# Kernel optimization log

Measured on AMD Instinct MI355X. Metric: run time of the kernel, lower is better.

## Reference

```python
import jax, jax.numpy as jnp
import numpy as np

H, W = 512, 512
N = H * W
NCLS = 4
D_BI, D_SP = 5, 2
THETA_ALPHA, THETA_BETA, THETA_GAMMA = 80.0, 0.0625, 3.0
BI_COMPAT, SP_COMPAT, COMPATIBILITY = 10.0, 3.0, -1.0
NUM_ITER = 10


def _build_lattice(feats):
    """Permutohedral lattice precompute (numpy, integer index construction).
    feats: [N, d]. Returns os [N,d+1] int32 (1-based), ws [N,d+1] float32,
    bn [d+1, M, 2] int32 (0 = missing neighbor), M."""
    feats = np.asarray(feats, np.float64)
    n, d = feats.shape
    inv_std = np.sqrt(2.0 / 3.0) * (d + 1)
    scale = inv_std / np.sqrt((np.arange(d) + 1.0) * (np.arange(d) + 2.0))
    cf = feats * scale
    # embedding matrix E: elevated = cf @ E.T lies on the hyperplane sum=0
    E = np.zeros((d + 1, d))
    E[0, :] = 1.0
    for j in range(1, d + 1):
        E[j, j:] = 1.0
        E[j, j - 1] = -j
    elevated = cf @ E.T  # [n, d+1]
    greedy = (np.rint(elevated / (d + 1)) * (d + 1)).astype(np.int64)
    diff = elevated - greedy
    idx = np.arange(d + 1)
    upper = idx[None, :] > idx[:, None]
    lower = idx[None, :] < idx[:, None]
    di = diff[:, :, None]
    dj = diff[:, None, :]
    rank = (((dj > di) & upper) | ((dj >= di) & lower)).sum(-1)
    rank = rank + greedy.sum(1, keepdims=True) // (d + 1)
    low = rank < 0
    rank = rank + np.where(low, d + 1, 0)
    greedy = greedy + np.where(low, d + 1, 0)
    high = rank > d
    rank = rank - np.where(high, d + 1, 0)
    greedy = greedy - np.where(high, d + 1, 0)
    # barycentric weights
    bary = np.zeros((n, d + 2))
    v = (elevated - greedy) / (d + 1)
    rows = np.repeat(np.arange(n), d + 1)
    np.add.at(bary, (rows, (d - rank).ravel()), v.ravel())
    np.add.at(bary, (rows, (d + 1 - rank).ravel()), -v.ravel())
    bary[:, 0] += 1.0 + bary[:, d + 1]
    ws = bary[:, : d + 1].astype(np.float32)
    # simplex vertex keys (first d coords; last is implied by zero-sum)
    keys = np.empty((n, d + 1, d), np.int64)
    for r in range(d + 1):
        keys[:, r, :] = (greedy + r - (d + 1) * (rank > d - r))[:, :d]
    flat = keys.reshape(-1, d)
    lo = flat.min(0) - (d + 1)
    hi = flat.max(0) + (d + 1)
    strides = np.cumprod(np.concatenate([[1], (hi - lo + 1)[:-1]]))
    coords = (flat - lo) @ strides
    uniq, first, inv = np.unique(coords, return_index=True, return_inverse=True)
    M = int(len(uniq))
    os_ = (inv.reshape(n, d + 1) + 1).astype(np.int32)
    ukeys = flat[first]
    bn = np.zeros((d + 1, M, 2), np.int32)
    for j in range(d + 1):
        n1 = ukeys - 1
        n2 = ukeys + 1
        if j < d:
            n1[:, j] = ukeys[:, j] + d
            n2[:, j] = ukeys[:, j] - d
        for t, nk in enumerate((n1, n2)):
            c = (nk - lo) @ strides
            pos = np.clip(np.searchsorted(uniq, c), 0, M - 1)
            bn[j, :, t] = np.where(uniq[pos] == c, pos + 1, 0)
    return os_, ws, bn, M


def setup_inputs() -> dict:
    key = jax.random.key(0)
    k1, k2 = jax.random.split(key)
    image = jax.random.uniform(k1, (H, W, 7), dtype=jnp.float32)
    unary = jax.random.normal(k2, (H, W, NCLS), dtype=jnp.float32)
    img = np.asarray(image)
    yy, xx = np.mgrid[0:H, 0:W].astype(np.float64)
    bifeat = np.concatenate(
        [(xx / THETA_ALPHA)[..., None], (yy / THETA_ALPHA)[..., None],
         img[..., :3] / THETA_BETA], axis=-1).reshape(N, D_BI)
    spfeat = np.stack([xx / THETA_GAMMA, yy / THETA_GAMMA], -1).reshape(N, D_SP)
    os_b, ws_b, bn_b, M_b = _build_lattice(bifeat)
    os_s, ws_s, bn_s, M_s = _build_lattice(spfeat)
    return {
        "unary": unary,
        "ws_bilateral": jnp.asarray(ws_b), "os_bilateral": jnp.asarray(os_b),
        "blur_neighbors_bilateral": jnp.asarray(bn_b), "M_bilateral": M_b,
        "ws_spatial": jnp.asarray(ws_s), "os_spatial": jnp.asarray(os_s),
        "blur_neighbors_spatial": jnp.asarray(bn_s), "M_spatial": M_s,
    }


def _perm_filter(values, os_, ws, bn, M, alpha):
    # values: [N, C]; splat -> blur -> slice
    d1 = os_.shape[1]
    C = values.shape[1]
    table = jnp.zeros((M + 1, C), values.dtype)  # row 0 = dummy (missing)
    table = table.at[os_.reshape(-1)].add(
        (values[:, None, :] * ws[:, :, None]).reshape(-1, C))
    for j in range(d1):  # [0.5, 1, 0.5] blur along each lattice axis
        table = table.at[1:].add(0.5 * (table[bn[j, :, 0]] + table[bn[j, :, 1]]))
    return alpha * jnp.einsum("nrc,nr->nc", table[os_], ws)


def _mean_field(unary, ws_b, os_b, bn_b, M_b, ws_s, os_s, bn_s, M_s):
    C = unary.shape[-1]
    u = unary.reshape(N, C)
    alpha_b = 1.0 / (1.0 + 2.0 ** (-D_BI))
    alpha_s = 1.0 / (1.0 + 2.0 ** (-D_SP))
    ones = jnp.ones((N, 1), u.dtype)
    inv_nb = 1.0 / (_perm_filter(ones, os_b, ws_b, bn_b, M_b, alpha_b) + 1e-20)
    inv_ns = 1.0 / (_perm_filter(ones, os_s, ws_s, bn_s, M_s, alpha_s) + 1e-20)
    Q = jax.nn.softmax(-u, axis=-1)
    for _ in range(NUM_ITER):
        msg = (BI_COMPAT * _perm_filter(Q, os_b, ws_b, bn_b, M_b, alpha_b) * inv_nb
               + SP_COMPAT * _perm_filter(Q, os_s, ws_s, bn_s, M_s, alpha_s) * inv_ns)
        Q = jax.nn.softmax(-u - COMPATIBILITY * msg, axis=-1)
    return Q.reshape(H, W, C)


def reference(unary, ws_bilateral, os_bilateral, blur_neighbors_bilateral, M_bilateral,
              ws_spatial, os_spatial, blur_neighbors_spatial, M_spatial):
    # Returns the refined marginals Q [H, W, NCLS]; the module's MAP output is
    # jnp.argmax(Q, -1) (kept soft here so fwd/bwd share one output).
    return _mean_field(unary, ws_bilateral, os_bilateral, blur_neighbors_bilateral,
                       M_bilateral, ws_spatial, os_spatial, blur_neighbors_spatial,
                       M_spatial)
```

## Files before the change

kernel.cpp:

```cpp
#include <hip/hip_runtime.h>

#define NPIX (512 * 512)
#define BLK 256

#define TOTB (NPIX * 6)
#define TOTS (NPIX * 3)
#define TOTE (NPIX * 9)

typedef unsigned long long u64;

constexpr float ALPHA_B = 32.0f / 33.0f;
constexpr float ALPHA_S = 0.8f;
constexpr float BI_COMPAT = 10.0f;
constexpr float SP_COMPAT = 3.0f;

__device__ __forceinline__ unsigned pack_ent(int n, float w) {
    float wc = fminf(fmaxf(w, 0.f), 1.f);
    unsigned iw = (unsigned)(wc * 16383.f + 0.5f);
    return (iw << 18) | (unsigned)n;
}
__device__ __forceinline__ int ent_pix(unsigned e) { return (int)(e & 0x3FFFFu); }
__device__ __forceinline__ float ent_w(unsigned e) {
    return (float)(e >> 18) * (1.0f / 16383.0f);
}
__device__ __forceinline__ u64 mknode(int nxt, unsigned pay) {
    return ((u64)(unsigned)nxt << 32) | (u64)pay;
}

__device__ __forceinline__ float4 f4zero() { return make_float4(0.f, 0.f, 0.f, 0.f); }

__global__ void k_softmax_init(const float4* __restrict__ u, float4* __restrict__ Q) {
    int n = blockIdx.x * BLK + threadIdx.x;
    if (n >= NPIX) return;
    float4 uu = u[n];
    float l0 = -uu.x, l1 = -uu.y, l2 = -uu.z, l3 = -uu.w;
    float m = fmaxf(fmaxf(l0, l1), fmaxf(l2, l3));
    float e0 = expf(l0 - m), e1 = expf(l1 - m), e2 = expf(l2 - m), e3 = expf(l3 - m);
    float inv = 1.0f / (e0 + e1 + e2 + e3);
    Q[n] = make_float4(e0 * inv, e1 * inv, e2 * inv, e3 * inv);
}

__global__ void k_link2_softmax(const int* __restrict__ osb, const float* __restrict__ wsb,
                                const int* __restrict__ oss, const float* __restrict__ wss,
                                int* __restrict__ head, u64* __restrict__ next2,
                                const float4* __restrict__ u, float4* __restrict__ Q,
                                int Vb) {
    int n = blockIdx.x * BLK + threadIdx.x;
    float4 uu = u[n];
    float l0 = -uu.x, l1 = -uu.y, l2 = -uu.z, l3 = -uu.w;
    float m = fmaxf(fmaxf(l0, l1), fmaxf(l2, l3));
    float e0 = expf(l0 - m), e1 = expf(l1 - m), e2 = expf(l2 - m), e3 = expf(l3 - m);
    float inv = 1.0f / (e0 + e1 + e2 + e3);
    Q[n] = make_float4(e0 * inv, e1 * inv, e2 * inv, e3 * inv);
#pragma unroll
    for (int r = 0; r < 6; r++) {
        int o = osb[n * 6 + r];
        int e = n * 6 + r;
        int old = atomicExch(&head[o], e);
        next2[e] = mknode(old, pack_ent(n, wsb[n * 6 + r]));
    }
#pragma unroll
    for (int r = 0; r < 3; r++) {
        int o = Vb + oss[n * 3 + r];
        int e = TOTB + n * 3 + r;
        int old = atomicExch(&head[o], e);
        next2[e] = mknode(old, pack_ent(n, wss[n * 3 + r]));
    }
}

__global__ void k_compact2(const int* __restrict__ head, const u64* __restrict__ next2,
                           unsigned* __restrict__ ent, int* __restrict__ start,
                           int* __restrict__ endv,
                           float* __restrict__ nB, float* __restrict__ nS,
                           int* __restrict__ cursor, int V, int Vb) {
    __shared__ int lds[BLK];
    __shared__ int sbase;
    int o = blockIdx.x * BLK + threadIdx.x;
    bool valid = o < V;
    int h = valid ? head[o] : -1;
    int len = 0;
    for (int e = h; e >= 0;) { e = (int)(next2[e] >> 32); len++; }
    lds[threadIdx.x] = len;
    __syncthreads();
    for (int off = 1; off < BLK; off <<= 1) {
        int t = ((int)threadIdx.x >= off) ? lds[threadIdx.x - off] : 0;
        __syncthreads();
        lds[threadIdx.x] += t;
        __syncthreads();
    }
    int incl = lds[threadIdx.x];
    if (threadIdx.x == BLK - 1) sbase = atomicAdd(cursor, incl);
    __syncthreads();
    if (!valid) return;
    int pos = sbase + incl - len;
    start[o] = pos;
    endv[o] = pos + len;
    float acc = 0.f;
    for (int e = h; e >= 0;) {
        u64 nd = next2[e];
        unsigned pe = (unsigned)nd;
        acc += ent_w(pe);
        ent[pos++] = pe;
        e = (int)(nd >> 32);
    }
    if (o < Vb) nB[o] = acc;
    else nS[o - Vb] = acc;
}

__global__ void k_link_softmax(const int* __restrict__ osb, const int* __restrict__ oss,
                               int* __restrict__ head, int* __restrict__ next,
                               const float4* __restrict__ u, float4* __restrict__ Q,
                               int Vb) {
    int n = blockIdx.x * BLK + threadIdx.x;
    if (n >= NPIX) return;
    float4 uu = u[n];
    float l0 = -uu.x, l1 = -uu.y, l2 = -uu.z, l3 = -uu.w;
    float m = fmaxf(fmaxf(l0, l1), fmaxf(l2, l3));
    float e0 = expf(l0 - m), e1 = expf(l1 - m), e2 = expf(l2 - m), e3 = expf(l3 - m);
    float inv = 1.0f / (e0 + e1 + e2 + e3);
    Q[n] = make_float4(e0 * inv, e1 * inv, e2 * inv, e3 * inv);
#pragma unroll
    for (int r = 0; r < 6; r++) {
        int o = osb[n * 6 + r];
        int e = n * 6 + r;
        next[e] = atomicExch(&head[o], e);
    }
#pragma unroll
    for (int r = 0; r < 3; r++) {
        int o = Vb + oss[n * 3 + r];
        int e = TOTB + n * 3 + r;
        next[e] = atomicExch(&head[o], e);
    }
}

__global__ void k_compact(const int* __restrict__ head, const int* __restrict__ next,
                          const float* __restrict__ wsb, const float* __restrict__ wss,
                          unsigned* __restrict__ ent, int* __restrict__ start,
                          int* __restrict__ endv,
                          float* __restrict__ nB, float* __restrict__ nS,
                          int* __restrict__ cursor, int V, int Vb) {
    __shared__ int lds[BLK];
    __shared__ int sbase;
    int o = blockIdx.x * BLK + threadIdx.x;
    bool valid = o < V;
    int h = valid ? head[o] : -1;
    int len = 0;
    for (int e = h; e >= 0; e = next[e]) len++;
    lds[threadIdx.x] = len;
    __syncthreads();
    for (int off = 1; off < BLK; off <<= 1) {
        int t = ((int)threadIdx.x >= off) ? lds[threadIdx.x - off] : 0;
        __syncthreads();
        lds[threadIdx.x] += t;
        __syncthreads();
    }
    int incl = lds[threadIdx.x];
    if (threadIdx.x == BLK - 1) sbase = atomicAdd(cursor, incl);
    __syncthreads();
    if (!valid) return;
    int pos = sbase + incl - len;
    start[o] = pos;
    endv[o] = pos + len;
    float acc = 0.f;
    if (o < Vb) {
        for (int e = h; e >= 0; e = next[e]) {
            unsigned n = (unsigned)e / 6u;
            unsigned pe = pack_ent((int)n, wsb[e]);
            acc += ent_w(pe);
            ent[pos++] = pe;
        }
        nB[o] = acc;
    } else {
        for (int e = h; e >= 0; e = next[e]) {
            int ee = e - TOTB;
            unsigned pe = pack_ent(ee / 3, wss[ee]);
            acc += ent_w(pe);
            ent[pos++] = pe;
        }
        nS[o - Vb] = acc;
    }
}

__global__ void k_compose(const int* __restrict__ bnb, int Mb, int Vb,
                          const int* __restrict__ bns, int Ms, int Vs,
                          int* __restrict__ cidxB, int* __restrict__ cidxS) {
    int t = blockIdx.x * BLK + threadIdx.x;
    int TB = 3 * Vb;
    const int* bnj; const int* bnk; int* c; int i, V;
    if (t < TB) {
        int p = t / Vb;
        i = t - p * Vb;
        if (i == 0) return;
        bnj = bnb + (size_t)(2 * p) * Mb * 2;
        bnk = bnb + (size_t)(2 * p + 1) * Mb * 2;
        c = cidxB + (size_t)p * 8 * Vb;
        V = Vb;
    } else {
        i = t - TB;
        if (i >= Vs || i == 0) return;
        bnj = bns;
        bnk = bns + (size_t)Ms * 2;
        c = cidxS;
        V = Vs;
    }
    int A = bnk[(size_t)(i - 1) * 2 + 0];
    int B = bnk[(size_t)(i - 1) * 2 + 1];
    int a1 = bnj[(size_t)(i - 1) * 2 + 0];
    int a2 = bnj[(size_t)(i - 1) * 2 + 1];
    int A1 = 0, A2 = 0, B1 = 0, B2 = 0;
    if (A > 0) { A1 = bnj[(size_t)(A - 1) * 2 + 0]; A2 = bnj[(size_t)(A - 1) * 2 + 1]; }
    if (B > 0) { B1 = bnj[(size_t)(B - 1) * 2 + 0]; B2 = bnj[(size_t)(B - 1) * 2 + 1]; }
    c[0 * (size_t)V + i] = a1;
    c[1 * (size_t)V + i] = a2;
    c[2 * (size_t)V + i] = A;
    c[3 * (size_t)V + i] = A1;
    c[4 * (size_t)V + i] = A2;
    c[5 * (size_t)V + i] = B;
    c[6 * (size_t)V + i] = B1;
    c[7 * (size_t)V + i] = B2;
}

__device__ __forceinline__ void blur2f4_core(const float4* __restrict__ in, float4* __restrict__ out,
                                             const int* __restrict__ c, int V, int i) {
    if (i == 0) { out[0] = f4zero(); return; }
    int a1 = c[0 * (size_t)V + i], a2 = c[1 * (size_t)V + i];
    int A  = c[2 * (size_t)V + i], A1 = c[3 * (size_t)V + i], A2 = c[4 * (size_t)V + i];
    int B  = c[5 * (size_t)V + i], B1 = c[6 * (size_t)V + i], B2 = c[7 * (size_t)V + i];
    float4 vi = in[i], va1 = in[a1], va2 = in[a2];
    float4 vA = in[A], vA1 = in[A1], vA2 = in[A2];
    float4 vB = in[B], vB1 = in[B1], vB2 = in[B2];
    float4 o;
    o.x = vi.x + 0.5f * (va1.x + va2.x + vA.x + vB.x) + 0.25f * (vA1.x + vA2.x + vB1.x + vB2.x);
    o.y = vi.y + 0.5f * (va1.y + va2.y + vA.y + vB.y) + 0.25f * (vA1.y + vA2.y + vB1.y + vB2.y);
    o.z = vi.z + 0.5f * (va1.z + va2.z + vA.z + vB.z) + 0.25f * (vA1.z + vA2.z + vB1.z + vB2.z);
    o.w = vi.w + 0.5f * (va1.w + va2.w + vA.w + vB.w) + 0.25f * (vA1.w + vA2.w + vB1.w + vB2.w);
    out[i] = o;
}

__device__ __forceinline__ void blur2f_core(const float* __restrict__ in, float* __restrict__ out,
                                            const int* __restrict__ c, int V, int i) {
    if (i == 0) { out[0] = 0.f; return; }
    int a1 = c[0 * (size_t)V + i], a2 = c[1 * (size_t)V + i];
    int A  = c[2 * (size_t)V + i], A1 = c[3 * (size_t)V + i], A2 = c[4 * (size_t)V + i];
    int B  = c[5 * (size_t)V + i], B1 = c[6 * (size_t)V + i], B2 = c[7 * (size_t)V + i];
    out[i] = in[i] + 0.5f * (in[a1] + in[a2] + in[A] + in[B])
                   + 0.25f * (in[A1] + in[A2] + in[B1] + in[B2]);
}

__device__ __forceinline__ void blur1f4_core(const float4* __restrict__ in, float4* __restrict__ out,
                                             const int* __restrict__ bn, int i) {
    if (i == 0) { out[0] = f4zero(); return; }
    int n1 = bn[(size_t)(i - 1) * 2 + 0];
    int n2 = bn[(size_t)(i - 1) * 2 + 1];
    float4 a = in[i], b = in[n1], c = in[n2];
    out[i] = make_float4(a.x + 0.5f * (b.x + c.x), a.y + 0.5f * (b.y + c.y),
                         a.z + 0.5f * (b.z + c.z), a.w + 0.5f * (b.w + c.w));
}

__global__ void k_blur2f4_both(const float4* __restrict__ inB, float4* __restrict__ outB,
                               const int* __restrict__ cB, int Vb,
                               const float4* __restrict__ inS, float4* __restrict__ outS,
                               const int* __restrict__ cS, int Vs) {
    int i = blockIdx.x * BLK + threadIdx.x;
    if (i < Vb) blur2f4_core(inB, outB, cB, Vb, i);
    else if (i - Vb < Vs) blur2f4_core(inS, outS, cS, Vs, i - Vb);
}
__global__ void k_blur2f4_b1s(const float4* __restrict__ inB, float4* __restrict__ outB,
                              const int* __restrict__ cB, int Vb,
                              const float4* __restrict__ inS, float4* __restrict__ outS,
                              const int* __restrict__ bnS, int Vs) {
    int i = blockIdx.x * BLK + threadIdx.x;
    if (i < Vb) blur2f4_core(inB, outB, cB, Vb, i);
    else if (i - Vb < Vs) blur1f4_core(inS, outS, bnS, i - Vb);
}
__global__ void k_blur2f4_b(const float4* __restrict__ inB, float4* __restrict__ outB,
                            const int* __restrict__ cB, int Vb) {
    int i = blockIdx.x * BLK + threadIdx.x;
    if (i < Vb) blur2f4_core(inB, outB, cB, Vb, i);
}
__global__ void k_blur2f_both(const float* __restrict__ inB, float* __restrict__ outB,
                              const int* __restrict__ cB, int Vb,
                              const float* __restrict__ inS, float* __restrict__ outS,
                              const int* __restrict__ cS, int Vs) {
    int i = blockIdx.x * BLK + threadIdx.x;
    if (i < Vb) blur2f_core(inB, outB, cB, Vb, i);
    else if (i - Vb < Vs) blur2f_core(inS, outS, cS, Vs, i - Vb);
}
__global__ void k_blur2f_b1s(const float* __restrict__ inB, float* __restrict__ outB,
                             const int* __restrict__ cB, int Vb,
                             const float* __restrict__ inS, float* __restrict__ outS,
                             const int* __restrict__ bnS, int Vs) {
    int i = blockIdx.x * BLK + threadIdx.x;
    if (i < Vb) blur2f_core(inB, outB, cB, Vb, i);
    else if (i - Vb < Vs) {
        int idx = i - Vb;
        if (idx == 0) { outS[0] = 0.f; return; }
        int n1 = bnS[(size_t)(idx - 1) * 2 + 0];
        int n2 = bnS[(size_t)(idx - 1) * 2 + 1];
        outS[idx] = inS[idx] + 0.5f * (inS[n1] + inS[n2]);
    }
}
__global__ void k_blur2f_b(const float* __restrict__ inB, float* __restrict__ outB,
                           const int* __restrict__ cB, int Vb) {
    int i = blockIdx.x * BLK + threadIdx.x;
    if (i < Vb) blur2f_core(inB, outB, cB, Vb, i);
}

__global__ void k_gather4f_both(const unsigned* __restrict__ ent, const int* __restrict__ start,
                                const int* __restrict__ endv, int V, int Vb,
                                float4* __restrict__ tB, float4* __restrict__ tS,
                                const float4* __restrict__ Q) {
    int i = blockIdx.x * BLK + threadIdx.x;
    if (i >= V) return;
    int s = start[i];
    int e = endv[i];
    float ax = 0.f, ay = 0.f, az = 0.f, aw = 0.f;
    for (int k = s; k < e; k++) {
        unsigned en = ent[k];
        float w = ent_w(en);
        float4 q = Q[ent_pix(en)];
        ax += w * q.x; ay += w * q.y; az += w * q.z; aw += w * q.w;
    }
    float4 h = make_float4(ax, ay, az, aw);
    if (i < Vb) tB[i] = h;
    else tS[i - Vb] = h;
}

__global__ void k_blur1(const float* __restrict__ in, float* __restrict__ out,
                        const int* __restrict__ bn, int M) {
    int i = blockIdx.x * BLK + threadIdx.x;
    if (i > M) return;
    if (i == 0) { out[0] = 0.f; return; }
    int n1 = bn[(size_t)(i - 1) * 2 + 0];
    int n2 = bn[(size_t)(i - 1) * 2 + 1];
    out[i] = in[i] + 0.5f * (in[n1] + in[n2]);
}

__global__ void k_blur1_both(const float* __restrict__ inB, float* __restrict__ outB,
                             const int* __restrict__ bnB, int Mb,
                             const float* __restrict__ inS, float* __restrict__ outS,
                             const int* __restrict__ bnS, int Ms) {
    int i = blockIdx.x * BLK + threadIdx.x;
    const float* in; float* out; const int* bn; int M, idx;
    if (i <= Mb) { in = inB; out = outB; bn = bnB; M = Mb; idx = i; }
    else {
        idx = i - (Mb + 1);
        if (idx > Ms) return;
        in = inS; out = outS; bn = bnS; M = Ms;
    }
    if (idx == 0) { out[0] = 0.f; return; }
    int n1 = bn[(size_t)(idx - 1) * 2 + 0];
    int n2 = bn[(size_t)(idx - 1) * 2 + 1];
    out[idx] = in[idx] + 0.5f * (in[n1] + in[n2]);
}

__global__ void k_blur4(const float4* __restrict__ in, float4* __restrict__ out,
                        const int* __restrict__ bn, int M) {
    int i = blockIdx.x * BLK + threadIdx.x;
    if (i > M) return;
    blur1f4_core(in, out, bn, i);
}

__global__ void k_blur4_both(const float4* __restrict__ inB, float4* __restrict__ outB,
                             const int* __restrict__ bnB, int Mb,
                             const float4* __restrict__ inS, float4* __restrict__ outS,
                             const int* __restrict__ bnS, int Ms) {
    int i = blockIdx.x * BLK + threadIdx.x;
    if (i <= Mb) blur1f4_core(inB, outB, bnB, i);
    else if (i - (Mb + 1) <= Ms) blur1f4_core(inS, outS, bnS, i - (Mb + 1));
}

__global__ void k_norm_prescale(const float* __restrict__ nTb, const float* __restrict__ wsb,
                                const int* __restrict__ osb,
                                const float* __restrict__ nTs, const float* __restrict__ wss,
                                const int* __restrict__ oss,
                                float* __restrict__ wsbp, float* __restrict__ wssp) {
    int n = blockIdx.x * BLK + threadIdx.x;
    if (n >= NPIX) return;
    float sb = 0.f;
#pragma unroll
    for (int r = 0; r < 6; r++) sb += wsb[n * 6 + r] * nTb[osb[n * 6 + r]];
    float cb = BI_COMPAT * ALPHA_B / (ALPHA_B * sb + 1e-20f);
#pragma unroll
    for (int r = 0; r < 6; r++) wsbp[n * 6 + r] = wsb[n * 6 + r] * cb;
    float ss = 0.f;
#pragma unroll
    for (int r = 0; r < 3; r++) ss += wss[n * 3 + r] * nTs[oss[n * 3 + r]];
    float cs = SP_COMPAT * ALPHA_S / (ALPHA_S * ss + 1e-20f);
#pragma unroll
    for (int r = 0; r < 3; r++) wssp[n * 3 + r] = wss[n * 3 + r] * cs;
}

__global__ void k_slice_combine_f(const float4* __restrict__ u,
                                  const float4* __restrict__ tb, const float* __restrict__ wsbp,
                                  const int* __restrict__ osb,
                                  const float4* __restrict__ ts, const float* __restrict__ wssp,
                                  const int* __restrict__ oss,
                                  float4* __restrict__ Qout) {
    int n = blockIdx.x * BLK + threadIdx.x;
    if (n >= NPIX) return;
    float4 uu = u[n];
    float l0 = -uu.x, l1 = -uu.y, l2 = -uu.z, l3 = -uu.w;
#pragma unroll
    for (int r = 0; r < 6; r++) {
        float w = wsbp[n * 6 + r];
        float4 t = tb[osb[n * 6 + r]];
        l0 += w * t.x; l1 += w * t.y; l2 += w * t.z; l3 += w * t.w;
    }
#pragma unroll
    for (int r = 0; r < 3; r++) {
        float w = wssp[n * 3 + r];
        float4 t = ts[oss[n * 3 + r]];
        l0 += w * t.x; l1 += w * t.y; l2 += w * t.z; l3 += w * t.w;
    }
    float m = fmaxf(fmaxf(l0, l1), fmaxf(l2, l3));
    float e0 = expf(l0 - m), e1 = expf(l1 - m), e2 = expf(l2 - m), e3 = expf(l3 - m);
    float inv = 1.0f / (e0 + e1 + e2 + e3);
    Qout[n] = make_float4(e0 * inv, e1 * inv, e2 * inv, e3 * inv);
}

template <int D1>
__global__ void k_splat1(const float* __restrict__ ws, const int* __restrict__ os,
                         float* __restrict__ table) {
    int n = blockIdx.x * BLK + threadIdx.x;
    if (n >= NPIX) return;
#pragma unroll
    for (int r = 0; r < D1; r++) atomicAdd(&table[os[n * D1 + r]], ws[n * D1 + r]);
}

template <int D1>
__global__ void k_splat4(const float4* __restrict__ Q, const float* __restrict__ ws,
                         const int* __restrict__ os, float* __restrict__ table) {
    int n = blockIdx.x * BLK + threadIdx.x;
    if (n >= NPIX) return;
    float4 q = Q[n];
#pragma unroll
    for (int r = 0; r < D1; r++) {
        float w = ws[n * D1 + r];
        int o = os[n * D1 + r];
        float* t = table + 4 * (size_t)o;
        atomicAdd(t + 0, q.x * w);
        atomicAdd(t + 1, q.y * w);
        atomicAdd(t + 2, q.z * w);
        atomicAdd(t + 3, q.w * w);
    }
}

template <int D1>
__global__ void k_norm_slice(const float* __restrict__ table, const float* __restrict__ ws,
                             const int* __restrict__ os, float alpha,
                             float* __restrict__ inv_out) {
    int n = blockIdx.x * BLK + threadIdx.x;
    if (n >= NPIX) return;
    float s = 0.f;
#pragma unroll
    for (int r = 0; r < D1; r++) s += ws[n * D1 + r] * table[os[n * D1 + r]];
    inv_out[n] = 1.0f / (alpha * s + 1e-20f);
}

__global__ void k_slice_combine(const float4* __restrict__ u,
                                const float4* __restrict__ tb, const float* __restrict__ wsb,
                                const int* __restrict__ osb,
                                const float4* __restrict__ ts, const float* __restrict__ wss,
                                const int* __restrict__ oss,
                                const float* __restrict__ inv_nb,
                                const float* __restrict__ inv_ns,
                                float4* __restrict__ Qout) {
    int n = blockIdx.x * BLK + threadIdx.x;
    if (n >= NPIX) return;
    float4 ab = f4zero();
#pragma unroll
    for (int r = 0; r < 6; r++) {
        float w = wsb[n * 6 + r];
        float4 t = tb[osb[n * 6 + r]];
        ab.x += w * t.x; ab.y += w * t.y; ab.z += w * t.z; ab.w += w * t.w;
    }
    float4 as = f4zero();
#pragma unroll
    for (int r = 0; r < 3; r++) {
        float w = wss[n * 3 + r];
        float4 t = ts[oss[n * 3 + r]];
        as.x += w * t.x; as.y += w * t.y; as.z += w * t.z; as.w += w * t.w;
    }
    float cb = BI_COMPAT * ALPHA_B * inv_nb[n];
    float cs = SP_COMPAT * ALPHA_S * inv_ns[n];
    float4 uu = u[n];
    float l0 = -uu.x + cb * ab.x + cs * as.x;
    float l1 = -uu.y + cb * ab.y + cs * as.y;
    float l2 = -uu.z + cb * ab.z + cs * as.z;
    float l3 = -uu.w + cb * ab.w + cs * as.w;
    float m = fmaxf(fmaxf(l0, l1), fmaxf(l2, l3));
    float e0 = expf(l0 - m), e1 = expf(l1 - m), e2 = expf(l2 - m), e3 = expf(l3 - m);
    float inv = 1.0f / (e0 + e1 + e2 + e3);
    Qout[n] = make_float4(e0 * inv, e1 * inv, e2 * inv, e3 * inv);
}

extern "C" void kernel_launch(void* const* d_in, const int* in_sizes, int n_in,
                              void* d_out, int out_size, void* d_ws, size_t ws_size,
                              hipStream_t stream) {
    const float* unary = (const float*)d_in[0];
    const float* wsb   = (const float*)d_in[1];
    const int*   osb   = (const int*)d_in[2];
    const int*   bnb   = (const int*)d_in[3];
    const float* wss   = (const float*)d_in[5];
    const int*   oss   = (const int*)d_in[6];
    const int*   bns   = (const int*)d_in[7];
    const int Mb = in_sizes[3] / 12;
    const int Ms = in_sizes[7] / 6;
    const int Vb = Mb + 1, Vs = Ms + 1;
    const int V = Vb + Vs;

    float* Q = (float*)d_out;

    char* p = (char*)d_ws;
    auto alloc = [&](size_t nbytes) -> void* {
        void* r = (void*)p;
        p += (nbytes + 15) & ~(size_t)15;
        return r;
    };
    char* region0 = p;
    float* wsbp = (float*)alloc((size_t)NPIX * 6 * 4);
    float* wssp = (float*)alloc((size_t)NPIX * 3 * 4);
    float4* tAb = (float4*)alloc((size_t)Vb * 16);
    float4* tBb = (float4*)alloc((size_t)Vb * 16);
    float4* tAs = (float4*)alloc((size_t)Vs * 16);
    float4* tBs = (float4*)alloc((size_t)Vs * 16);
    float* nBb = (float*)alloc((size_t)Vb * 4);
    float* nBs = (float*)alloc((size_t)Vs * 4);
    float* nAb = (float*)alloc((size_t)Vb * 4);
    float* nAs = (float*)alloc((size_t)Vs * 4);
    int*  start = (int*)alloc((size_t)V * 4);
    int*  endv  = (int*)alloc((size_t)V * 4);
    int*  head  = (int*)alloc((size_t)V * 4);
    unsigned* ent = (unsigned*)alloc((size_t)TOTE * 4);
    int*  cursor = (int*)alloc(16);
    size_t base_need = (size_t)(p - (char*)d_ws);
    u64*  next2 = (u64*)alloc((size_t)TOTE * 8);
    size_t need8 = (size_t)(p - (char*)d_ws);
    int* cidxB = (int*)alloc((size_t)Vb * 8 * 3 * 4);
    int* cidxS = (int*)alloc((size_t)Vs * 8 * 4);
    size_t need_fused = (size_t)(p - (char*)d_ws);
    bool use_gather = base_need <= ws_size;
    bool use8 = need8 <= ws_size;
    bool use_fused = need_fused <= ws_size;
    int*  next4 = (int*)region0;

    dim3 blk(BLK);
    dim3 gN((NPIX + BLK - 1) / BLK);
    dim3 gVb((Vb + BLK - 1) / BLK);
    dim3 gV((V + BLK - 1) / BLK);
    dim3 gVBS((Vb + Vs + BLK - 1) / BLK);
    dim3 gC((3 * Vb + Vs + BLK - 1) / BLK);

    if (use_gather) {
        hipMemsetAsync(head, 0xFF, (size_t)V * 4, stream);
        hipMemsetAsync(cursor, 0, 16, stream);
        if (use_fused)
            k_compose<<<gC, blk, 0, stream>>>(bnb, Mb, Vb, bns, Ms, Vs, cidxB, cidxS);
        if (use8) {
            k_link2_softmax<<<gN, blk, 0, stream>>>(osb, wsb, oss, wss, head, next2,
                                                    (const float4*)unary, (float4*)Q, Vb);
            k_compact2<<<gV, blk, 0, stream>>>(head, next2, ent, start, endv,
                                               nAb, nAs, cursor, V, Vb);
        } else {
            k_link_softmax<<<gN, blk, 0, stream>>>(osb, oss, head, next4,
                                                   (const float4*)unary, (float4*)Q, Vb);
            k_compact<<<gV, blk, 0, stream>>>(head, next4, wsb, wss, ent, start, endv,
                                              nAb, nAs, cursor, V, Vb);
        }

        const int* cB01 = cidxB;
        const int* cB23 = cidxB + (size_t)1 * 8 * Vb;
        const int* cB45 = cidxB + (size_t)2 * 8 * Vb;
        const int* bnS2 = bns + (size_t)2 * Ms * 2;

        if (use_fused) {
            k_blur2f_both<<<gVBS, blk, 0, stream>>>(nAb, nBb, cB01, Vb, nAs, nBs, cidxS, Vs);
            k_blur2f_b1s<<<gVBS, blk, 0, stream>>>(nBb, nAb, cB23, Vb, nBs, nAs, bnS2, Vs);
            k_blur2f_b<<<gVb, blk, 0, stream>>>(nAb, nBb, cB45, Vb);
            k_norm_prescale<<<gN, blk, 0, stream>>>(nBb, wsb, osb, nAs, wss, oss, wsbp, wssp);
        } else {
            float* a = nAb; float* b = nBb;
            float* as_ = nAs; float* bs_ = nBs;
            for (int j = 0; j < 3; j++) {
                k_blur1_both<<<gVBS, blk, 0, stream>>>(a, b, bnb + (size_t)j * Mb * 2, Mb,
                                                       as_, bs_, bns + (size_t)j * Ms * 2, Ms);
                float* t = a; a = b; b = t;
                t = as_; as_ = bs_; bs_ = t;
            }
            for (int j = 3; j < 6; j++) {
                k_blur1<<<gVb, blk, 0, stream>>>(a, b, bnb + (size_t)j * Mb * 2, Mb);
                float* t = a; a = b; b = t;
            }
            k_norm_prescale<<<gN, blk, 0, stream>>>(a, wsb, osb, as_, wss, oss, wsbp, wssp);
        }

        for (int it = 0; it < 10; it++) {
            k_gather4f_both<<<gV, blk, 0, stream>>>(ent, start, endv, V, Vb, tAb, tAs,
                                                    (const float4*)Q);
            if (use_fused) {
                k_blur2f4_both<<<gVBS, blk, 0, stream>>>(tAb, tBb, cB01, Vb, tAs, tBs, cidxS, Vs);
                k_blur2f4_b1s<<<gVBS, blk, 0, stream>>>(tBb, tAb, cB23, Vb, tBs, tAs, bnS2, Vs);
                k_blur2f4_b<<<gVb, blk, 0, stream>>>(tAb, tBb, cB45, Vb);
                k_slice_combine_f<<<gN, blk, 0, stream>>>((const float4*)unary,
                                                          tBb, wsbp, osb, tAs, wssp, oss,
                                                          (float4*)Q);
            } else {
                float4* a = tAb; float4* b = tBb;
                float4* as_ = tAs; float4* bs_ = tBs;
                for (int j = 0; j < 3; j++) {
                    k_blur4_both<<<gVBS, blk, 0, stream>>>(a, b, bnb + (size_t)j * Mb * 2, Mb,
                                                           as_, bs_, bns + (size_t)j * Ms * 2, Ms);
                    float4* t = a; a = b; b = t;
                    t = as_; as_ = bs_; bs_ = t;
                }
                for (int j = 3; j < 6; j++) {
                    k_blur4<<<gVb, blk, 0, stream>>>(a, b, bnb + (size_t)j * Mb * 2, Mb);
                    float4* t = a; a = b; b = t;
                }
                k_slice_combine_f<<<gN, blk, 0, stream>>>((const float4*)unary,
                                                          a, wsbp, osb, as_, wssp, oss,
                                                          (float4*)Q);
            }
        }
    } else {
        char* q = (char*)d_ws;
        auto alloc2 = [&](size_t nbytes) -> void* {
            void* r = (void*)q;
            q += (nbytes + 15) & ~(size_t)15;
            return r;
        };
        float* fAb = (float*)alloc2((size_t)Vb * 4 * sizeof(float));
        float* fBb = (float*)alloc2((size_t)Vb * 4 * sizeof(float));
        float* fAs = (float*)alloc2((size_t)Vs * 4 * sizeof(float));
        float* fBs = (float*)alloc2((size_t)Vs * 4 * sizeof(float));
        float* inv_nb = (float*)alloc2(NPIX * sizeof(float));
        float* inv_ns = (float*)alloc2(NPIX * sizeof(float));
        dim3 gMb((Mb + 1 + BLK - 1) / BLK);
        dim3 gMs((Ms + 1 + BLK - 1) / BLK);

        hipMemsetAsync(fAb, 0, (size_t)Vb * sizeof(float), stream);
        k_splat1<6><<<gN, blk, 0, stream>>>(wsb, osb, fAb);
        {
            float* a = fAb; float* b = fBb;
            for (int j = 0; j < 6; j++) {
                k_blur1<<<gMb, blk, 0, stream>>>(a, b, bnb + (size_t)j * Mb * 2, Mb);
                float* t = a; a = b; b = t;
            }
            k_norm_slice<6><<<gN, blk, 0, stream>>>(a, wsb, osb, ALPHA_B, inv_nb);
        }
        hipMemsetAsync(fAs, 0, (size_t)Vs * sizeof(float), stream);
        k_splat1<3><<<gN, blk, 0, stream>>>(wss, oss, fAs);
        {
            float* a = fAs; float* b = fBs;
            for (int j = 0; j < 3; j++) {
                k_blur1<<<gMs, blk, 0, stream>>>(a, b, bns + (size_t)j * Ms * 2, Ms);
                float* t = a; a = b; b = t;
            }
            k_norm_slice<3><<<gN, blk, 0, stream>>>(a, wss, oss, ALPHA_S, inv_ns);
        }
        k_softmax_init<<<gN, blk, 0, stream>>>((const float4*)unary, (float4*)Q);
        for (int it = 0; it < 10; it++) {
            hipMemsetAsync(fAb, 0, (size_t)Vb * 4 * sizeof(float), stream);
            k_splat4<6><<<gN, blk, 0, stream>>>((const float4*)Q, wsb, osb, fAb);
            float* a = fAb; float* b = fBb;
            for (int j = 0; j < 6; j++) {
                k_blur4<<<gMb, blk, 0, stream>>>((const float4*)a, (float4*)b,
                                                 bnb + (size_t)j * Mb * 2, Mb);
                float* t = a; a = b; b = t;
            }
            float* finb = a;
            hipMemsetAsync(fAs, 0, (size_t)Vs * 4 * sizeof(float), stream);
            k_splat4<3><<<gN, blk, 0, stream>>>((const float4*)Q, wss, oss, fAs);
            float* as_ = fAs; float* bs_ = fBs;
            for (int j = 0; j < 3; j++) {
                k_blur4<<<gMs, blk, 0, stream>>>((const float4*)as_, (float4*)bs_,
                                                 bns + (size_t)j * Ms * 2, Ms);
                float* t = as_; as_ = bs_; bs_ = t;
            }
            float* fins = as_;
            k_slice_combine<<<gN, blk, 0, stream>>>((const float4*)unary,
                                                    (const float4*)finb, wsb, osb,
                                                    (const float4*)fins, wss, oss,
                                                    inv_nb, inv_ns, (float4*)Q);
        }
    }
}
```

Before: 935.5 us.

## Split spatial-lattice gather across four lanes and pack slice weights with offsets

The spatial-lattice part of the splat gather now uses four threads per vertex. Their partial sums are combined with wavefront shuffles, which spreads the long per-vertex entry lists of the coarse spatial lattice over more lanes. Start and end offsets are merged into one int2 array. Prescaled slice weights are stored interleaved with their lattice offsets so each slice tap needs one 8-byte load. The next2 linked-list buffer now aliases the prescaled-weight region, and the 4-byte-next fallback path is removed. This reuse of workspace memory assumes the lifetimes do not overlap and that the workspace is large enough.

```diff
diff --git a/kernel.cpp b/kernel.cpp
--- a/kernel.cpp
+++ b/kernel.cpp
@@ -69,8 +69,7 @@
 }
 
 __global__ void k_compact2(const int* __restrict__ head, const u64* __restrict__ next2,
-                           unsigned* __restrict__ ent, int* __restrict__ start,
-                           int* __restrict__ endv,
+                           unsigned* __restrict__ ent, int2* __restrict__ se,
                            float* __restrict__ nB, float* __restrict__ nS,
                            int* __restrict__ cursor, int V, int Vb) {
     __shared__ int lds[BLK];
@@ -93,8 +92,7 @@
     __syncthreads();
     if (!valid) return;
     int pos = sbase + incl - len;
-    start[o] = pos;
-    endv[o] = pos + len;
+    se[o] = make_int2(pos, pos + len);
     float acc = 0.f;
     for (int e = h; e >= 0;) {
         u64 nd = next2[e];
@@ -105,80 +103,6 @@
     }
     if (o < Vb) nB[o] = acc;
     else nS[o - Vb] = acc;
-}
-
-__global__ void k_link_softmax(const int* __restrict__ osb, const int* __restrict__ oss,
-                               int* __restrict__ head, int* __restrict__ next,
-                               const float4* __restrict__ u, float4* __restrict__ Q,
-                               int Vb) {
-    int n = blockIdx.x * BLK + threadIdx.x;
-    if (n >= NPIX) return;
-    float4 uu = u[n];
-    float l0 = -uu.x, l1 = -uu.y, l2 = -uu.z, l3 = -uu.w;
-    float m = fmaxf(fmaxf(l0, l1), fmaxf(l2, l3));
-    float e0 = expf(l0 - m), e1 = expf(l1 - m), e2 = expf(l2 - m), e3 = expf(l3 - m);
-    float inv = 1.0f / (e0 + e1 + e2 + e3);
-    Q[n] = make_float4(e0 * inv, e1 * inv, e2 * inv, e3 * inv);
-#pragma unroll
-    for (int r = 0; r < 6; r++) {
-        int o = osb[n * 6 + r];
-        int e = n * 6 + r;
-        next[e] = atomicExch(&head[o], e);
-    }
-#pragma unroll
-    for (int r = 0; r < 3; r++) {
-        int o = Vb + oss[n * 3 + r];
-        int e = TOTB + n * 3 + r;
-        next[e] = atomicExch(&head[o], e);
-    }
-}
-
-__global__ void k_compact(const int* __restrict__ head, const int* __restrict__ next,
-                          const float* __restrict__ wsb, const float* __restrict__ wss,
-                          unsigned* __restrict__ ent, int* __restrict__ start,
-                          int* __restrict__ endv,
-                          float* __restrict__ nB, float* __restrict__ nS,
-                          int* __restrict__ cursor, int V, int Vb) {
-    __shared__ int lds[BLK];
-    __shared__ int sbase;
-    int o = blockIdx.x * BLK + threadIdx.x;
-    bool valid = o < V;
-    int h = valid ? head[o] : -1;
-    int len = 0;
-    for (int e = h; e >= 0; e = next[e]) len++;
-    lds[threadIdx.x] = len;
-    __syncthreads();
-    for (int off = 1; off < BLK; off <<= 1) {
-        int t = ((int)threadIdx.x >= off) ? lds[threadIdx.x - off] : 0;
-        __syncthreads();
-        lds[threadIdx.x] += t;
-        __syncthreads();
-    }
-    int incl = lds[threadIdx.x];
-    if (threadIdx.x == BLK - 1) sbase = atomicAdd(cursor, incl);
-    __syncthreads();
-    if (!valid) return;
-    int pos = sbase + incl - len;
-    start[o] = pos;
-    endv[o] = pos + len;
-    float acc = 0.f;
-    if (o < Vb) {
-        for (int e = h; e >= 0; e = next[e]) {
-            unsigned n = (unsigned)e / 6u;
-            unsigned pe = pack_ent((int)n, wsb[e]);
-            acc += ent_w(pe);
-            ent[pos++] = pe;
-        }
-        nB[o] = acc;
-    } else {
-        for (int e = h; e >= 0; e = next[e]) {
-            int ee = e - TOTB;
-            unsigned pe = pack_ent(ee / 3, wss[ee]);
-            acc += ent_w(pe);
-            ent[pos++] = pe;
-        }
-        nS[o - Vb] = acc;
-    }
 }
 
 __global__ void k_compose(const int* __restrict__ bnb, int Mb, int Vb,
@@ -306,24 +230,41 @@
     if (i < Vb) blur2f_core(inB, outB, cB, Vb, i);
 }
 
-__global__ void k_gather4f_both(const unsigned* __restrict__ ent, const int* __restrict__ start,
-                                const int* __restrict__ endv, int V, int Vb,
+__global__ void k_gather4f_both(const unsigned* __restrict__ ent, const int2* __restrict__ se,
+                                int Vb, int Vb4, int Vs,
                                 float4* __restrict__ tB, float4* __restrict__ tS,
                                 const float4* __restrict__ Q) {
     int i = blockIdx.x * BLK + threadIdx.x;
-    if (i >= V) return;
-    int s = start[i];
-    int e = endv[i];
+    if (i < Vb) {
+        int2 r = se[i];
+        float ax = 0.f, ay = 0.f, az = 0.f, aw = 0.f;
+        for (int k = r.x; k < r.y; k++) {
+            unsigned en = ent[k];
+            float w = ent_w(en);
+            float4 q = Q[ent_pix(en)];
+            ax += w * q.x; ay += w * q.y; az += w * q.z; aw += w * q.w;
+        }
+        tB[i] = make_float4(ax, ay, az, aw);
+        return;
+    }
+    if (i < Vb4) return;
+    int j = i - Vb4;
+    int v = j >> 2;
+    if (v >= Vs) return;
+    int sub = j & 3;
+    int2 r = se[Vb + v];
     float ax = 0.f, ay = 0.f, az = 0.f, aw = 0.f;
-    for (int k = s; k < e; k++) {
+    for (int k = r.x + sub; k < r.y; k += 4) {
         unsigned en = ent[k];
         float w = ent_w(en);
         float4 q = Q[ent_pix(en)];
         ax += w * q.x; ay += w * q.y; az += w * q.z; aw += w * q.w;
     }
-    float4 h = make_float4(ax, ay, az, aw);
-    if (i < Vb) tB[i] = h;
-    else tS[i - Vb] = h;
+    ax += __shfl_xor(ax, 1); ay += __shfl_xor(ay, 1);
+    az += __shfl_xor(az, 1); aw += __shfl_xor(aw, 1);
+    ax += __shfl_xor(ax, 2); ay += __shfl_xor(ay, 2);
+    az += __shfl_xor(az, 2); aw += __shfl_xor(aw, 2);
+    if (sub == 0) tS[v] = make_float4(ax, ay, az, aw);
 }
 
 __global__ void k_blur1(const float* __restrict__ in, float* __restrict__ out,
@@ -374,7 +315,7 @@
                                 const int* __restrict__ osb,
                                 const float* __restrict__ nTs, const float* __restrict__ wss,
                                 const int* __restrict__ oss,
-                                float* __restrict__ wsbp, float* __restrict__ wssp) {
+                                int2* __restrict__ pwb, int2* __restrict__ pws) {
     int n = blockIdx.x * BLK + threadIdx.x;
     if (n >= NPIX) return;
     float sb = 0.f;
@@ -382,20 +323,20 @@
     for (int r = 0; r < 6; r++) sb += wsb[n * 6 + r] * nTb[osb[n * 6 + r]];
     float cb = BI_COMPAT * ALPHA_B / (ALPHA_B * sb + 1e-20f);
 #pragma unroll
-    for (int r = 0; r < 6; r++) wsbp[n * 6 + r] = wsb[n * 6 + r] * cb;
+    for (int r = 0; r < 6; r++)
+        pwb[n * 6 + r] = make_int2(__float_as_int(wsb[n * 6 + r] * cb), osb[n * 6 + r]);
     float ss = 0.f;
 #pragma unroll
     for (int r = 0; r < 3; r++) ss += wss[n * 3 + r] * nTs[oss[n * 3 + r]];
     float cs = SP_COMPAT * ALPHA_S / (ALPHA_S * ss + 1e-20f);
 #pragma unroll
-    for (int r = 0; r < 3; r++) wssp[n * 3 + r] = wss[n * 3 + r] * cs;
+    for (int r = 0; r < 3; r++)
+        pws[n * 3 + r] = make_int2(__float_as_int(wss[n * 3 + r] * cs), oss[n * 3 + r]);
 }
 
 __global__ void k_slice_combine_f(const float4* __restrict__ u,
-                                  const float4* __restrict__ tb, const float* __restrict__ wsbp,
-                                  const int* __restrict__ osb,
-                                  const float4* __restrict__ ts, const float* __restrict__ wssp,
-                                  const int* __restrict__ oss,
+                                  const float4* __restrict__ tb, const int2* __restrict__ pwb,
+                                  const float4* __restrict__ ts, const int2* __restrict__ pws,
                                   float4* __restrict__ Qout) {
     int n = blockIdx.x * BLK + threadIdx.x;
     if (n >= NPIX) return;
@@ -403,14 +344,16 @@
     float l0 = -uu.x, l1 = -uu.y, l2 = -uu.z, l3 = -uu.w;
 #pragma unroll
     for (int r = 0; r < 6; r++) {
-        float w = wsbp[n * 6 + r];
-        float4 t = tb[osb[n * 6 + r]];
+        int2 p = pwb[n * 6 + r];
+        float w = __int_as_float(p.x);
+        float4 t = tb[p.y];
         l0 += w * t.x; l1 += w * t.y; l2 += w * t.z; l3 += w * t.w;
     }
 #pragma unroll
     for (int r = 0; r < 3; r++) {
-        float w = wssp[n * 3 + r];
-        float4 t = ts[oss[n * 3 + r]];
+        int2 p = pws[n * 3 + r];
+        float w = __int_as_float(p.x);
+        float4 t = ts[p.y];
         l0 += w * t.x; l1 += w * t.y; l2 += w * t.z; l3 += w * t.w;
     }
     float m = fmaxf(fmaxf(l0, l1), fmaxf(l2, l3));
@@ -509,6 +452,7 @@
     const int Ms = in_sizes[7] / 6;
     const int Vb = Mb + 1, Vs = Ms + 1;
     const int V = Vb + Vs;
+    const int Vb4 = (Vb + 3) & ~3;
 
     float* Q = (float*)d_out;
 
@@ -519,36 +463,33 @@
         return r;
     };
     char* region0 = p;
-    float* wsbp = (float*)alloc((size_t)NPIX * 6 * 4);
-    float* wssp = (float*)alloc((size_t)NPIX * 3 * 4);
+    int2* pwb = (int2*)alloc((size_t)TOTB * 8);
+    int2* pws = (int2*)alloc((size_t)TOTS * 8);
     float4* tAb = (float4*)alloc((size_t)Vb * 16);
     float4* tBb = (float4*)alloc((size_t)Vb * 16);
     float4* tAs = (float4*)alloc((size_t)Vs * 16);
     float4* tBs = (float4*)alloc((size_t)Vs * 16);
     float* nBb = (float*)alloc((size_t)Vb * 4);
     float* nBs = (float*)alloc((size_t)Vs * 4);
+    u64*  next2 = (u64*)region0;
     float* nAb = (float*)alloc((size_t)Vb * 4);
     float* nAs = (float*)alloc((size_t)Vs * 4);
-    int*  start = (int*)alloc((size_t)V * 4);
-    int*  endv  = (int*)alloc((size_t)V * 4);
-    int*  head  = (int*)alloc((size_t)V * 4);
+    int2* se   = (int2*)alloc((size_t)V * 8);
+    int*  head = (int*)alloc((size_t)V * 4);
     unsigned* ent = (unsigned*)alloc((size_t)TOTE * 4);
     int*  cursor = (int*)alloc(16);
     size_t base_need = (size_t)(p - (char*)d_ws);
-    u64*  next2 = (u64*)alloc((size_t)TOTE * 8);
-    size_t need8 = (size_t)(p - (char*)d_ws);
     int* cidxB = (int*)alloc((size_t)Vb * 8 * 3 * 4);
     int* cidxS = (int*)alloc((size_t)Vs * 8 * 4);
     size_t need_fused = (size_t)(p - (char*)d_ws);
     bool use_gather = base_need <= ws_size;
-    bool use8 = need8 <= ws_size;
     bool use_fused = need_fused <= ws_size;
-    int*  next4 = (int*)region0;
 
     dim3 blk(BLK);
     dim3 gN((NPIX + BLK - 1) / BLK);
     dim3 gVb((Vb + BLK - 1) / BLK);
     dim3 gV((V + BLK - 1) / BLK);
+    dim3 gG((Vb4 + 4 * Vs + BLK - 1) / BLK);
     dim3 gVBS((Vb + Vs + BLK - 1) / BLK);
     dim3 gC((3 * Vb + Vs + BLK - 1) / BLK);
 
@@ -557,17 +498,9 @@
         hipMemsetAsync(cursor, 0, 16, stream);
         if (use_fused)
             k_compose<<<gC, blk, 0, stream>>>(bnb, Mb, Vb, bns, Ms, Vs, cidxB, cidxS);
-        if (use8) {
-            k_link2_softmax<<<gN, blk, 0, stream>>>(osb, wsb, oss, wss, head, next2,
-                                                    (const float4*)unary, (float4*)Q, Vb);
-            k_compact2<<<gV, blk, 0, stream>>>(head, next2, ent, start, endv,
-                                               nAb, nAs, cursor, V, Vb);
-        } else {
-            k_link_softmax<<<gN, blk, 0, stream>>>(osb, oss, head, next4,
-                                                   (const float4*)unary, (float4*)Q, Vb);
-            k_compact<<<gV, blk, 0, stream>>>(head, next4, wsb, wss, ent, start, endv,
-                                              nAb, nAs, cursor, V, Vb);
-        }
+        k_link2_softmax<<<gN, blk, 0, stream>>>(osb, wsb, oss, wss, head, next2,
+                                                (const float4*)unary, (float4*)Q, Vb);
+        k_compact2<<<gV, blk, 0, stream>>>(head, next2, ent, se, nAb, nAs, cursor, V, Vb);
 
         const int* cB01 = cidxB;
         const int* cB23 = cidxB + (size_t)1 * 8 * Vb;
@@ -578,7 +511,7 @@
             k_blur2f_both<<<gVBS, blk, 0, stream>>>(nAb, nBb, cB01, Vb, nAs, nBs, cidxS, Vs);
             k_blur2f_b1s<<<gVBS, blk, 0, stream>>>(nBb, nAb, cB23, Vb, nBs, nAs, bnS2, Vs);
             k_blur2f_b<<<gVb, blk, 0, stream>>>(nAb, nBb, cB45, Vb);
-            k_norm_prescale<<<gN, blk, 0, stream>>>(nBb, wsb, osb, nAs, wss, oss, wsbp, wssp);
+            k_norm_prescale<<<gN, blk, 0, stream>>>(nBb, wsb, osb, nAs, wss, oss, pwb, pws);
         } else {
             float* a = nAb; float* b = nBb;
             float* as_ = nAs; float* bs_ = nBs;
@@ -592,19 +525,18 @@
                 k_blur1<<<gVb, blk, 0, stream>>>(a, b, bnb + (size_t)j * Mb * 2, Mb);
                 float* t = a; a = b; b = t;
             }
-            k_norm_prescale<<<gN, blk, 0, stream>>>(a, wsb, osb, as_, wss, oss, wsbp, wssp);
+            k_norm_prescale<<<gN, blk, 0, stream>>>(a, wsb, osb, as_, wss, oss, pwb, pws);
         }
 
         for (int it = 0; it < 10; it++) {
-            k_gather4f_both<<<gV, blk, 0, stream>>>(ent, start, endv, V, Vb, tAb, tAs,
+            k_gather4f_both<<<gG, blk, 0, stream>>>(ent, se, Vb, Vb4, Vs, tAb, tAs,
                                                     (const float4*)Q);
             if (use_fused) {
                 k_blur2f4_both<<<gVBS, blk, 0, stream>>>(tAb, tBb, cB01, Vb, tAs, tBs, cidxS, Vs);
                 k_blur2f4_b1s<<<gVBS, blk, 0, stream>>>(tBb, tAb, cB23, Vb, tBs, tAs, bnS2, Vs);
                 k_blur2f4_b<<<gVb, blk, 0, stream>>>(tAb, tBb, cB45, Vb);
                 k_slice_combine_f<<<gN, blk, 0, stream>>>((const float4*)unary,
-                                                          tBb, wsbp, osb, tAs, wssp, oss,
-                                                          (float4*)Q);
+                                                          tBb, pwb, tAs, pws, (float4*)Q);
             } else {
                 float4* a = tAb; float4* b = tBb;
                 float4* as_ = tAs; float4* bs_ = tBs;
@@ -619,8 +551,7 @@
                     float4* t = a; a = b; b = t;
                 }
                 k_slice_combine_f<<<gN, blk, 0, stream>>>((const float4*)unary,
-                                                          a, wsbp, osb, as_, wssp, oss,
-                                                          (float4*)Q);
+                                                          a, pwb, as_, pws, (float4*)Q);
             }
         }
     } else {
```

Result: faster. 869.8 us (-7.0%).
